# Kernel optimization log

Hardware: AMD Instinct MI355X
Metric: run time of the kernel (lower is better)

Reference implementation:

```python
import jax, jax.numpy as jnp
import numpy as np

EMBED_DIM = 1024
NUM_HEADS = 16
BATCH = 4
SEQ = 2048
HEAD_DIM = EMBED_DIM // NUM_HEADS


def get_alibi_slope(num_heads):
    x = (2 ** 8) ** (1 / num_heads)
    slope = jnp.array([1 / x ** (i + 1) for i in range(num_heads)], dtype=jnp.float32)
    return slope[:, None, None]  # [H,1,1]


def setup_inputs() -> dict:
    key = jax.random.key(0)
    k1, k2, k3 = jax.random.split(key, 3)
    x = jax.random.normal(k1, (BATCH, SEQ, EMBED_DIM), dtype=jnp.float32)
    # causal mask, broadcastable to [B,H,S,S]
    mask = jnp.tril(jnp.ones((SEQ, SEQ), dtype=bool))[None, None, :, :]
    W_qkv = jax.random.normal(k2, (EMBED_DIM, 3 * EMBED_DIM), dtype=jnp.float32) * (EMBED_DIM ** -0.5)
    b_qkv = jnp.zeros((3 * EMBED_DIM,), dtype=jnp.float32)
    W_out = jax.random.normal(k3, (EMBED_DIM, EMBED_DIM), dtype=jnp.float32) * (EMBED_DIM ** -0.5)
    b_out = jnp.zeros((EMBED_DIM,), dtype=jnp.float32)
    return {"x": x, "mask": mask, "W_qkv": W_qkv, "b_qkv": b_qkv, "W_out": W_out, "b_out": b_out}


def reference(x, mask, W_qkv, b_qkv, W_out, b_out):
    B, S, E = x.shape
    H, D = NUM_HEADS, HEAD_DIM
    qkv = x @ W_qkv + b_qkv                     # [B,S,3E]
    qkv = qkv.reshape(B, S, 3, H, D)
    q, k, v = qkv[:, :, 0], qkv[:, :, 1], qkv[:, :, 2]  # each [B,S,H,D]
    scores = jnp.einsum('bqhd,bkhd->bhqk', q, k) / jnp.sqrt(jnp.asarray(D, x.dtype))
    # ALiBi bias: slope[h] * (k_pos - q_pos)
    rel = (jnp.arange(S)[None, :] - jnp.arange(S)[:, None]).astype(x.dtype)  # [S,S]
    scores = scores + get_alibi_slope(H).astype(x.dtype) * rel               # broadcast [H,S,S]
    scores = jnp.where(mask, scores, jnp.asarray(-1e9, x.dtype))
    attn = jax.nn.softmax(scores, axis=-1)       # [B,H,S,S]
    out = jnp.einsum('bhqk,bkhd->bqhd', attn, v).reshape(B, S, E)
    return out @ W_out + b_out
```

## Files before the change

### kernel.cpp

```cpp
#include <hip/hip_runtime.h>
#include <hip/hip_bf16.h>
#include <cstdint>
#include <cstddef>

#define BATCH  4
#define SEQ    2048
#define EMBED  1024
#define NHEADS 16
#define HDIM   64

typedef __attribute__((ext_vector_type(8))) short  short8;
typedef __attribute__((ext_vector_type(4))) float  floatx4;

#define MASK_NEG (-1.0e30f)
#define LOG2E    1.44269504f

__device__ __forceinline__ float bf2f(ushort u) {
  union { uint32_t i; float f; } v; v.i = ((uint32_t)u) << 16; return v.f;
}
__device__ __forceinline__ ushort f2bf(float f) {
  union { float f; uint32_t i; } v; v.f = f;
  uint32_t u = v.i;
  return (ushort)((u + 0x7fffu + ((u >> 16) & 1u)) >> 16);
}
__device__ __forceinline__ uint32_t f2bf_pk(float a, float b) {
  union { __hip_bfloat162 h; uint32_t u; } v;
  v.h = __float22bfloat162_rn(make_float2(a, b));
  return v.u;
}
__device__ __forceinline__ float fast_exp2(float x) {
  float r;
  asm("v_exp_f32 %0, %1" : "=v"(r) : "v"(x));
  return r;
}
__device__ __forceinline__ floatx4 max4(floatx4 a, floatx4 b) {
  floatx4 r;
  r[0] = fmaxf(a[0], b[0]); r[1] = fmaxf(a[1], b[1]);
  r[2] = fmaxf(a[2], b[2]); r[3] = fmaxf(a[3], b[3]);
  return r;
}
__device__ __forceinline__ void gll16(const ushort* g, ushort* l) {
  __builtin_amdgcn_global_load_lds(
      (const __attribute__((address_space(1))) void*)g,
      (__attribute__((address_space(3))) void*)l, 16, 0, 0);
}

__global__ __launch_bounds__(256) void detect_dtype(
    const uint32_t* __restrict__ x, int* __restrict__ flag) {
  __shared__ int sh[256];
  int tid = threadIdx.x;
  int c = 0;
#pragma unroll
  for (int i = 0; i < 16; i++) {
    uint32_t w = x[tid * 16 + i];
    uint32_t lo = w & 0xFFFFu;
    int e = (int)((lo >> 7) & 0xFF);
    if (lo == 0u || (e >= 100 && e <= 140)) c++;
  }
  sh[tid] = c;
  __syncthreads();
  if (tid == 0) {
    int s = 0;
    for (int i = 0; i < 256; i++) s += sh[i];
    *flag = (s >= 3500) ? 1 : 0;
  }
}

__global__ __launch_bounds__(256) void cvt_bf16_v4(
    const void* __restrict__ in, ushort* __restrict__ out,
    const int* __restrict__ flag, int n4) {
  bool isbf = (*flag != 0);
  int stride = gridDim.x * 256;
  for (int i = blockIdx.x * 256 + threadIdx.x; i < n4; i += stride) {
    if (isbf) {
      ((uint2*)out)[i] = ((const uint2*)in)[i];
    } else {
      float4 f = ((const float4*)in)[i];
      uint2 o;
      o.x = f2bf_pk(f.x, f.y);
      o.y = f2bf_pk(f.z, f.w);
      ((uint2*)out)[i] = o;
    }
  }
}

__global__ __launch_bounds__(256) void cvt_biases(
    const void* __restrict__ bq, const void* __restrict__ bo,
    ushort* __restrict__ bqb, ushort* __restrict__ bob,
    const int* __restrict__ flag) {
  bool isbf = (*flag != 0);
  int i = blockIdx.x * 256 + threadIdx.x;
  if (i < 3 * EMBED) {
    bqb[i] = isbf ? ((const ushort*)bq)[i] : f2bf(((const float*)bq)[i]);
  } else {
    int j = i - 3 * EMBED;
    bob[j] = isbf ? ((const ushort*)bo)[j] : f2bf(((const float*)bo)[j]);
  }
}

__global__ __launch_bounds__(256) void transpose_cvt(
    const void* __restrict__ in, ushort* __restrict__ out,
    const int* __restrict__ flag, int R, int C) {
  bool isbf = (*flag != 0);
  __shared__ ushort tile[32][33];
  int bx = blockIdx.x * 32;
  int by = blockIdx.y * 32;
  int tx = threadIdx.x & 31, ty = threadIdx.x >> 5;
#pragma unroll
  for (int i = 0; i < 32; i += 8) {
    size_t idx = (size_t)(by + ty + i) * C + bx + tx;
    tile[ty + i][tx] = isbf ? ((const ushort*)in)[idx] : f2bf(((const float*)in)[idx]);
  }
  __syncthreads();
#pragma unroll
  for (int i = 0; i < 32; i += 8)
    out[(size_t)(bx + ty + i) * R + by + tx] = tile[tx][ty + i];
}

__global__ __launch_bounds__(256) void transpose_v(
    const ushort* __restrict__ in, ushort* __restrict__ out) {
  __shared__ ushort tile[32][33];
  int bh = blockIdx.z;
  int s0 = blockIdx.x * 32;
  int d0 = blockIdx.y * 32;
  int tx = threadIdx.x & 31, ty = threadIdx.x >> 5;
  const ushort* ip = in + (size_t)bh * SEQ * HDIM;
  ushort* op = out + (size_t)bh * SEQ * HDIM;
#pragma unroll
  for (int i = 0; i < 32; i += 8)
    tile[ty + i][tx] = ip[(size_t)(s0 + ty + i) * HDIM + d0 + tx];
  __syncthreads();
#pragma unroll
  for (int i = 0; i < 32; i += 8)
    op[(size_t)(d0 + ty + i) * SEQ + s0 + tx] = tile[tx][ty + i];
}

template <int EPI>
__global__ __launch_bounds__(256) void gemm128(
    const ushort* __restrict__ A, const ushort* __restrict__ BT,
    const ushort* __restrict__ bias,
    ushort* __restrict__ out0, ushort* __restrict__ out1, ushort* __restrict__ out2,
    const int* __restrict__ flag,
    int M, int N, int K) {
  __shared__ __align__(16) ushort Al[128 * 64];
  __shared__ __align__(16) ushort Bl[128 * 64];

  const int tid  = threadIdx.x;
  const int lane = tid & 63, wave = tid >> 6;
  const int quad = lane >> 4, l15 = lane & 15;
  const int wm = wave >> 1, wn = wave & 1;

  const int Lb  = blockIdx.y * gridDim.x + blockIdx.x;
  const int xcd = Lb & 7, ib = Lb >> 3;
  const int cpx = gridDim.x >> 3;
  const int bx  = xcd * cpx + (ib % cpx);
  const int by  = ib / cpx;
  const int rowA0 = by * 128;
  const int colB0 = bx * 128;

  floatx4 acc[4][4] = {};

  int srow[4], sc8[4];
#pragma unroll
  for (int j = 0; j < 4; j++) {
    int s = tid + j * 256;
    srow[j] = s >> 3;
    sc8[j] = ((s & 7) ^ (srow[j] & 7)) * 8;
  }

  for (int kk = 0; kk < K; kk += 64) {
    __syncthreads();
#pragma unroll
    for (int j = 0; j < 4; j++)
      gll16(&A[(size_t)(rowA0 + srow[j]) * K + kk + sc8[j]], &Al[(tid + j * 256) * 8]);
#pragma unroll
    for (int j = 0; j < 4; j++)
      gll16(&BT[(size_t)(colB0 + srow[j]) * K + kk + sc8[j]], &Bl[(tid + j * 256) * 8]);
    __syncthreads();

#pragma unroll
    for (int h = 0; h < 2; h++) {
      short8 af[4], bf[4];
#pragma unroll
      for (int mt = 0; mt < 4; mt++) {
        int row = wm * 64 + mt * 16 + l15;
        int pos = (quad + 4 * h) ^ (l15 & 7);
        af[mt] = *(const short8*)&Al[row * 64 + pos * 8];
      }
#pragma unroll
      for (int nt = 0; nt < 4; nt++) {
        int row = wn * 64 + nt * 16 + l15;
        int pos = (quad + 4 * h) ^ (l15 & 7);
        bf[nt] = *(const short8*)&Bl[row * 64 + pos * 8];
      }
#pragma unroll
      for (int mt = 0; mt < 4; mt++)
#pragma unroll
        for (int nt = 0; nt < 4; nt++)
          acc[mt][nt] = __builtin_amdgcn_mfma_f32_16x16x32_bf16(af[mt], bf[nt], acc[mt][nt], 0, 0, 0);
    }
  }

  const bool isbf = (EPI == 1) ? (*flag != 0) : true;

#pragma unroll
  for (int mt = 0; mt < 4; mt++)
#pragma unroll
    for (int nt = 0; nt < 4; nt++)
#pragma unroll
      for (int r = 0; r < 4; r++) {
        int row = rowA0 + wm * 64 + mt * 16 + quad * 4 + r;
        int col = colB0 + wn * 64 + nt * 16 + l15;
        float v = acc[mt][nt][r] + bf2f(bias[col]);
        if (EPI == 0) {
          int three = col >> 10, rem = col & 1023, h = rem >> 6, d = rem & 63;
          int b = row >> 11, s = row & 2047;
          ushort* dst = (three == 0) ? out0 : (three == 1) ? out1 : out2;
          dst[((size_t)(b * NHEADS + h) * SEQ + s) * HDIM + d] = f2bf(v);
        } else {
          if (isbf) out0[(size_t)row * N + col] = f2bf(v);
          else      ((float*)out0)[(size_t)row * N + col] = v;
        }
      }
}

__global__ __launch_bounds__(256, 3) void attn_kernel(
    const ushort* __restrict__ Q, const ushort* __restrict__ K,
    const ushort* __restrict__ VT, ushort* __restrict__ Oout) {
  __shared__ __align__(16) ushort Kl[2][64 * 64];
  __shared__ __align__(16) ushort Vt[2][64 * 64];
  __shared__ __align__(16) ushort Pl[4][32 * 64];

  const int tid  = threadIdx.x;
  const int lane = tid & 63, wave = tid >> 6;
  const int quad = lane >> 4, l15 = lane & 15;

  const int L   = blockIdx.x + 16 * blockIdx.y + 256 * blockIdx.z;
  const int xcd = L & 7;
  const int idx = L >> 3;
  const int bh  = xcd * 8 + (idx >> 4);
  const int qt  = 15 - (idx & 15);
  const int h   = bh & 15, b = bh >> 4;

  const ushort* Qp  = Q  + (size_t)bh * SEQ * HDIM;
  const ushort* Kp  = K  + (size_t)bh * SEQ * HDIM;
  const ushort* VTp = VT + (size_t)bh * SEQ * HDIM;

  const float slope2 = exp2f(-0.5f * (float)(h + 1)) * LOG2E;
  const float c2 = 0.125f * LOG2E;

  floatx4 ab[4];
#pragma unroll
  for (int kct = 0; kct < 4; kct++)
#pragma unroll
    for (int r = 0; r < 4; r++)
      ab[kct][r] = slope2 * (float)(kct * 16 + quad * 4 + r);

  const int sr0 = tid >> 3, sr1 = sr0 + 32;
  const int sc  = tid & 7;
  const int so  = sc * 8;
  const int sw0 = sr0 * 64 + (sc ^ (sr0 & 7)) * 8;
  const int sw1 = sr1 * 64 + (sc ^ (sr0 & 7)) * 8;
  const int sxr = l15 & 7;

  const int wq0 = qt * 128 + wave * 32;

  short8 qf[2][2];
#pragma unroll
  for (int mf = 0; mf < 2; mf++) {
    const ushort* qr = &Qp[(size_t)(wq0 + mf * 16 + l15) * HDIM];
    qf[mf][0] = *(const short8*)&qr[quad * 8];
    qf[mf][1] = *(const short8*)&qr[32 + quad * 8];
  }

  float m2s[2] = {MASK_NEG, MASK_NEG}, lis[2] = {0.f, 0.f};
  float qrowf[2];
#pragma unroll
  for (int mf = 0; mf < 2; mf++) qrowf[mf] = (float)(wq0 + mf * 16 + l15);
  floatx4 o_acc[2][4] = {};

#define ATTN_TILE(KB, CUR, MASKED)                                            \
  do {                                                                        \
    short8 kfa[4], kfb[4];                                                    \
    _Pragma("unroll")                                                         \
    for (int kct = 0; kct < 4; kct++) {                                       \
      const ushort* kr = &Kl[CUR][(kct * 16 + l15) * 64];                     \
      kfa[kct] = *(const short8*)&kr[(quad ^ sxr) * 8];                       \
      kfb[kct] = *(const short8*)&kr[((quad + 4) ^ sxr) * 8];                 \
    }                                                                         \
    _Pragma("unroll")                                                         \
    for (int mf = 0; mf < 2; mf++) {                                          \
      floatx4 w[4];                                                           \
      _Pragma("unroll")                                                       \
      for (int kct = 0; kct < 4; kct++) {                                     \
        floatx4 z = {};                                                       \
        z = __builtin_amdgcn_mfma_f32_16x16x32_bf16(kfa[kct], qf[mf][0], z, 0, 0, 0); \
        z = __builtin_amdgcn_mfma_f32_16x16x32_bf16(kfb[kct], qf[mf][1], z, 0, 0, 0); \
        w[kct] = z * c2 + ab[kct];                                            \
      }                                                                       \
      if (MASKED) {                                                           \
        const float qrel = qrowf[mf] - (float)(KB);                           \
        _Pragma("unroll")                                                     \
        for (int kct = 0; kct < 4; kct++)                                     \
          _Pragma("unroll")                                                   \
          for (int r = 0; r < 4; r++)                                         \
            if ((float)(kct * 16 + quad * 4 + r) > qrel) w[kct][r] = MASK_NEG;\
      }                                                                       \
      floatx4 wm4 = max4(max4(w[0], w[1]), max4(w[2], w[3]));                 \
      float mloc = fmaxf(fmaxf(wm4[0], wm4[1]), fmaxf(wm4[2], wm4[3]));       \
      mloc = fmaxf(mloc, __shfl_xor(mloc, 16, 64));                           \
      mloc = fmaxf(mloc, __shfl_xor(mloc, 32, 64));                           \
      const float bk = slope2 * (float)(KB);                                  \
      const float mlt = mloc + bk;                                            \
      const unsigned long long g = __ballot(mlt > m2s[mf] + 8.0f);            \
      float al = 1.0f;                                                        \
      if (g) {                                                                \
        float mn = fmaxf(m2s[mf], mlt);                                       \
        al = fast_exp2(m2s[mf] - mn);                                         \
        m2s[mf] = mn;                                                         \
      }                                                                       \
      const float mnb = m2s[mf] - bk;                                         \
      float rs = 0.f;                                                         \
      _Pragma("unroll")                                                       \
      for (int kct = 0; kct < 4; kct++) {                                     \
        float p0 = fast_exp2(w[kct][0] - mnb);                                \
        float p1 = fast_exp2(w[kct][1] - mnb);                                \
        float p2 = fast_exp2(w[kct][2] - mnb);                                \
        float p3 = fast_exp2(w[kct][3] - mnb);                                \
        rs += (p0 + p1) + (p2 + p3);                                          \
        uint2 pw;                                                             \
        pw.x = f2bf_pk(p0, p1);                                               \
        pw.y = f2bf_pk(p2, p3);                                               \
        *(uint2*)&Pl[wave][(mf * 16 + l15) * 64 +                             \
                           ((kct * 2 + (quad >> 1)) ^ sxr) * 8 +              \
                           (quad & 1) * 4] = pw;                              \
      }                                                                       \
      if (g) {                                                                \
        floatx4 alrv;                                                         \
        _Pragma("unroll")                                                     \
        for (int r = 0; r < 4; r++) alrv[r] = __shfl(al, quad * 4 + r, 16);   \
        _Pragma("unroll")                                                     \
        for (int ct = 0; ct < 4; ct++) o_acc[mf][ct] *= alrv;                 \
        lis[mf] = lis[mf] * al + rs;                                          \
      } else {                                                                \
        lis[mf] += rs;                                                        \
      }                                                                       \
    }                                                                         \
    _Pragma("unroll")                                                         \
    for (int ks = 0; ks < 2; ks++) {                                          \
      short8 vf[4];                                                           \
      _Pragma("unroll")                                                       \
      for (int ct = 0; ct < 4; ct++)                                          \
        vf[ct] = *(const short8*)&Vt[CUR][(ct * 16 + l15) * 64 +              \
                                          ((ks * 4 + quad) ^ sxr) * 8];       \
      _Pragma("unroll")                                                       \
      for (int mf = 0; mf < 2; mf++) {                                        \
        short8 pf = *(const short8*)&Pl[wave][(mf * 16 + l15) * 64 +          \
                                              ((ks * 4 + quad) ^ sxr) * 8];   \
        _Pragma("unroll")                                                     \
        for (int ct = 0; ct < 4; ct++)                                        \
          o_acc[mf][ct] = __builtin_amdgcn_mfma_f32_16x16x32_bf16(            \
              pf, vf[ct], o_acc[mf][ct], 0, 0, 0);                            \
      }                                                                       \
    }                                                                         \
  } while (0)

  uint4 pk0 = *(const uint4*)&Kp[(size_t)sr0 * HDIM + so];
  uint4 pk1 = *(const uint4*)&Kp[(size_t)sr1 * HDIM + so];
  uint4 pv0 = *(const uint4*)&VTp[(size_t)sr0 * SEQ + so];
  uint4 pv1 = *(const uint4*)&VTp[(size_t)sr1 * SEQ + so];
  *(uint4*)&Kl[0][sw0] = pk0;
  *(uint4*)&Kl[0][sw1] = pk1;
  *(uint4*)&Vt[0][sw0] = pv0;
  *(uint4*)&Vt[0][sw1] = pv1;
  __syncthreads();

  const int nfull = 2 * qt;
  for (int kt = 0; kt < nfull; kt++) {
    const int kb = kt * 64;
    const int cur = kt & 1;

    {
      const int kb2 = kb + 64;
      pk0 = *(const uint4*)&Kp[(size_t)(kb2 + sr0) * HDIM + so];
      pk1 = *(const uint4*)&Kp[(size_t)(kb2 + sr1) * HDIM + so];
      pv0 = *(const uint4*)&VTp[(size_t)sr0 * SEQ + kb2 + so];
      pv1 = *(const uint4*)&VTp[(size_t)sr1 * SEQ + kb2 + so];
    }

    ATTN_TILE(kb, cur, 0);

    {
      const int nxt = cur ^ 1;
      *(uint4*)&Kl[nxt][sw0] = pk0;
      *(uint4*)&Kl[nxt][sw1] = pk1;
      *(uint4*)&Vt[nxt][sw0] = pv0;
      *(uint4*)&Vt[nxt][sw1] = pv1;
    }
    __syncthreads();
  }

  {
    const int kb = nfull * 64;
    const int cur = nfull & 1;
    const int kb2 = kb + 64;
    pk0 = *(const uint4*)&Kp[(size_t)(kb2 + sr0) * HDIM + so];
    pk1 = *(const uint4*)&Kp[(size_t)(kb2 + sr1) * HDIM + so];
    pv0 = *(const uint4*)&VTp[(size_t)sr0 * SEQ + kb2 + so];
    pv1 = *(const uint4*)&VTp[(size_t)sr1 * SEQ + kb2 + so];

    ATTN_TILE(kb, cur, 1);

    const int nxt = cur ^ 1;
    *(uint4*)&Kl[nxt][sw0] = pk0;
    *(uint4*)&Kl[nxt][sw1] = pk1;
    *(uint4*)&Vt[nxt][sw0] = pv0;
    *(uint4*)&Vt[nxt][sw1] = pv1;
    __syncthreads();
  }

  if (wave & 2) {
    ATTN_TILE((nfull + 1) * 64, (nfull + 1) & 1, 1);
  }

#pragma unroll
  for (int mf = 0; mf < 2; mf++) {
    float lif = lis[mf] + __shfl_xor(lis[mf], 16, 64);
    lif += __shfl_xor(lif, 32, 64);
    float inv = 1.0f / fmaxf(lif, 1e-20f);
    float invr[4];
#pragma unroll
    for (int r = 0; r < 4; r++) invr[r] = __shfl(inv, quad * 4 + r, 16);
#pragma unroll
    for (int ct = 0; ct < 4; ct++)
#pragma unroll
      for (int r = 0; r < 4; r++) {
        int q = wq0 + mf * 16 + quad * 4 + r;
        float v = o_acc[mf][ct][r] * invr[r];
        Oout[(size_t)(b * SEQ + q) * EMBED + h * HDIM + ct * 16 + l15] = f2bf(v);
      }
  }
#undef ATTN_TILE
}

extern "C" void kernel_launch(void* const* d_in, const int* in_sizes, int n_in,
                              void* d_out, int out_size, void* d_ws, size_t ws_size,
                              hipStream_t stream) {
  const void* x     = d_in[0];
  const void* W_qkv = d_in[2];
  const void* b_qkv = d_in[3];
  const void* W_out = d_in[4];
  const void* b_out = d_in[5];

  char* ws = (char*)d_ws;
  int*    flag = (int*)(ws + 0);
  ushort* xb   = (ushort*)(ws + 1024);
  ushort* WTq  = (ushort*)(ws + 16778240);
  ushort* WTo  = (ushort*)(ws + 23069696);
  ushort* bqb  = (ushort*)(ws + 25166848);
  ushort* bob  = (ushort*)(ws + 25172992);
  ushort* Kw   = (ushort*)(ws + 25175040);
  ushort* Vw   = (ushort*)(ws + 41952256);
  ushort* VTw  = (ushort*)(ws + 58729472);
  ushort* Aw   = Vw;
  ushort* Qw   = (ws_size >= (size_t)75506688 + 16777216)
                   ? (ushort*)(ws + 75506688)
                   : (ushort*)d_out;

  detect_dtype<<<1, 256, 0, stream>>>((const uint32_t*)x, flag);

  cvt_bf16_v4<<<2048, 256, 0, stream>>>(x, xb, flag, BATCH * SEQ * EMBED / 4);
  cvt_biases<<<16, 256, 0, stream>>>(b_qkv, b_out, bqb, bob, flag);

  transpose_cvt<<<dim3(3072 / 32, 1024 / 32), 256, 0, stream>>>(W_qkv, WTq, flag, 1024, 3072);
  transpose_cvt<<<dim3(1024 / 32, 1024 / 32), 256, 0, stream>>>(W_out, WTo, flag, 1024, 1024);

  gemm128<0><<<dim3(3072 / 128, 8192 / 128), 256, 0, stream>>>(
      xb, WTq, bqb, Qw, Kw, Vw, flag, BATCH * SEQ, 3 * EMBED, EMBED);

  transpose_v<<<dim3(SEQ / 32, HDIM / 32, BATCH * NHEADS), 256, 0, stream>>>(Vw, VTw);

  attn_kernel<<<dim3(16, 16, 4), 256, 0, stream>>>(Qw, Kw, VTw, Aw);

  gemm128<1><<<dim3(1024 / 128, 8192 / 128), 256, 0, stream>>>(
      Aw, WTo, bob, (ushort*)d_out, nullptr, nullptr, flag, BATCH * SEQ, EMBED, EMBED);
}
```

Baseline: 328.8 us.

## Pair causal query tiles per block, stage K/V via direct global-to-LDS loads

The attention kernel now gives each block two query tiles (p and 15-p) so every block does the same amount of causal work, and halves the grid to 512 blocks. K/V staging switches from register prefetch plus LDS store to direct global-to-LDS loads (gll16), and launch bounds drop to 2 blocks per SM. The QKV/out GEMMs also drop the XCD-aware block swizzle in favour of plain blockIdx mapping. The aim is to remove tail imbalance from causal work and free registers. The costs are fewer resident blocks and possibly worse L2 locality in the GEMMs.

```diff
diff --git a/kernel.cpp b/kernel.cpp
--- a/kernel.cpp
+++ b/kernel.cpp
@@ -149,14 +149,8 @@
   const int lane = tid & 63, wave = tid >> 6;
   const int quad = lane >> 4, l15 = lane & 15;
   const int wm = wave >> 1, wn = wave & 1;
-
-  const int Lb  = blockIdx.y * gridDim.x + blockIdx.x;
-  const int xcd = Lb & 7, ib = Lb >> 3;
-  const int cpx = gridDim.x >> 3;
-  const int bx  = xcd * cpx + (ib % cpx);
-  const int by  = ib / cpx;
-  const int rowA0 = by * 128;
-  const int colB0 = bx * 128;
+  const int rowA0 = blockIdx.y * 128;
+  const int colB0 = blockIdx.x * 128;
 
   floatx4 acc[4][4] = {};
 
@@ -224,7 +218,7 @@
       }
 }
 
-__global__ __launch_bounds__(256, 3) void attn_kernel(
+__global__ __launch_bounds__(256, 2) void attn_kernel(
     const ushort* __restrict__ Q, const ushort* __restrict__ K,
     const ushort* __restrict__ VT, ushort* __restrict__ Oout) {
   __shared__ __align__(16) ushort Kl[2][64 * 64];
@@ -235,11 +229,11 @@
   const int lane = tid & 63, wave = tid >> 6;
   const int quad = lane >> 4, l15 = lane & 15;
 
-  const int L   = blockIdx.x + 16 * blockIdx.y + 256 * blockIdx.z;
+  const int L   = blockIdx.x + 8 * blockIdx.y + 128 * blockIdx.z;
   const int xcd = L & 7;
   const int idx = L >> 3;
-  const int bh  = xcd * 8 + (idx >> 4);
-  const int qt  = 15 - (idx & 15);
+  const int bh  = xcd * 8 + (idx >> 3);
+  const int p   = idx & 7;
   const int h   = bh & 15, b = bh >> 4;
 
   const ushort* Qp  = Q  + (size_t)bh * SEQ * HDIM;
@@ -256,28 +250,17 @@
     for (int r = 0; r < 4; r++)
       ab[kct][r] = slope2 * (float)(kct * 16 + quad * 4 + r);
 
-  const int sr0 = tid >> 3, sr1 = sr0 + 32;
-  const int sc  = tid & 7;
-  const int so  = sc * 8;
-  const int sw0 = sr0 * 64 + (sc ^ (sr0 & 7)) * 8;
-  const int sw1 = sr1 * 64 + (sc ^ (sr0 & 7)) * 8;
+  const int sr0 = tid >> 3;
+  const int scc = ((tid & 7) ^ (sr0 & 7)) * 8;
   const int sxr = l15 & 7;
 
-  const int wq0 = qt * 128 + wave * 32;
-
-  short8 qf[2][2];
-#pragma unroll
-  for (int mf = 0; mf < 2; mf++) {
-    const ushort* qr = &Qp[(size_t)(wq0 + mf * 16 + l15) * HDIM];
-    qf[mf][0] = *(const short8*)&qr[quad * 8];
-    qf[mf][1] = *(const short8*)&qr[32 + quad * 8];
-  }
-
-  float m2s[2] = {MASK_NEG, MASK_NEG}, lis[2] = {0.f, 0.f};
-  float qrowf[2];
-#pragma unroll
-  for (int mf = 0; mf < 2; mf++) qrowf[mf] = (float)(wq0 + mf * 16 + l15);
-  floatx4 o_acc[2][4] = {};
+#define STAGE(KB, BUF)                                                        \
+  do {                                                                        \
+    gll16(&Kp[(size_t)((KB) + sr0) * HDIM + scc],       &Kl[BUF][tid * 8]);   \
+    gll16(&Kp[(size_t)((KB) + sr0 + 32) * HDIM + scc],  &Kl[BUF][tid * 8 + 2048]); \
+    gll16(&VTp[(size_t)sr0 * SEQ + (KB) + scc],         &Vt[BUF][tid * 8]);   \
+    gll16(&VTp[(size_t)(sr0 + 32) * SEQ + (KB) + scc],  &Vt[BUF][tid * 8 + 2048]); \
+  } while (0)
 
 #define ATTN_TILE(KB, CUR, MASKED)                                            \
   do {                                                                        \
@@ -365,82 +348,67 @@
     }                                                                         \
   } while (0)
 
-  uint4 pk0 = *(const uint4*)&Kp[(size_t)sr0 * HDIM + so];
-  uint4 pk1 = *(const uint4*)&Kp[(size_t)sr1 * HDIM + so];
-  uint4 pv0 = *(const uint4*)&VTp[(size_t)sr0 * SEQ + so];
-  uint4 pv1 = *(const uint4*)&VTp[(size_t)sr1 * SEQ + so];
-  *(uint4*)&Kl[0][sw0] = pk0;
-  *(uint4*)&Kl[0][sw1] = pk1;
-  *(uint4*)&Vt[0][sw0] = pv0;
-  *(uint4*)&Vt[0][sw1] = pv1;
-  __syncthreads();
-
-  const int nfull = 2 * qt;
-  for (int kt = 0; kt < nfull; kt++) {
-    const int kb = kt * 64;
-    const int cur = kt & 1;
+  for (int qsel = 0; qsel < 2; qsel++) {
+    const int qt  = qsel ? (15 - p) : p;
+    const int wq0 = qt * 128 + wave * 32;
+
+    short8 qf[2][2];
+#pragma unroll
+    for (int mf = 0; mf < 2; mf++) {
+      const ushort* qr = &Qp[(size_t)(wq0 + mf * 16 + l15) * HDIM];
+      qf[mf][0] = *(const short8*)&qr[quad * 8];
+      qf[mf][1] = *(const short8*)&qr[32 + quad * 8];
+    }
+
+    float m2s[2] = {MASK_NEG, MASK_NEG}, lis[2] = {0.f, 0.f};
+    float qrowf[2];
+#pragma unroll
+    for (int mf = 0; mf < 2; mf++) qrowf[mf] = (float)(wq0 + mf * 16 + l15);
+    floatx4 o_acc[2][4] = {};
+
+    __syncthreads();
+    STAGE(0, 0);
+    __syncthreads();
+
+    const int nfull = 2 * qt;
+    for (int kt = 0; kt < nfull; kt++) {
+      const int cur = kt & 1;
+      STAGE((kt + 1) * 64, cur ^ 1);
+      ATTN_TILE(kt * 64, cur, 0);
+      __syncthreads();
+    }
 
     {
-      const int kb2 = kb + 64;
-      pk0 = *(const uint4*)&Kp[(size_t)(kb2 + sr0) * HDIM + so];
-      pk1 = *(const uint4*)&Kp[(size_t)(kb2 + sr1) * HDIM + so];
-      pv0 = *(const uint4*)&VTp[(size_t)sr0 * SEQ + kb2 + so];
-      pv1 = *(const uint4*)&VTp[(size_t)sr1 * SEQ + kb2 + so];
-    }
-
-    ATTN_TILE(kb, cur, 0);
-
-    {
-      const int nxt = cur ^ 1;
-      *(uint4*)&Kl[nxt][sw0] = pk0;
-      *(uint4*)&Kl[nxt][sw1] = pk1;
-      *(uint4*)&Vt[nxt][sw0] = pv0;
-      *(uint4*)&Vt[nxt][sw1] = pv1;
-    }
-    __syncthreads();
-  }
-
-  {
-    const int kb = nfull * 64;
-    const int cur = nfull & 1;
-    const int kb2 = kb + 64;
-    pk0 = *(const uint4*)&Kp[(size_t)(kb2 + sr0) * HDIM + so];
-    pk1 = *(const uint4*)&Kp[(size_t)(kb2 + sr1) * HDIM + so];
-    pv0 = *(const uint4*)&VTp[(size_t)sr0 * SEQ + kb2 + so];
-    pv1 = *(const uint4*)&VTp[(size_t)sr1 * SEQ + kb2 + so];
-
-    ATTN_TILE(kb, cur, 1);
-
-    const int nxt = cur ^ 1;
-    *(uint4*)&Kl[nxt][sw0] = pk0;
-    *(uint4*)&Kl[nxt][sw1] = pk1;
-    *(uint4*)&Vt[nxt][sw0] = pv0;
-    *(uint4*)&Vt[nxt][sw1] = pv1;
-    __syncthreads();
-  }
-
-  if (wave & 2) {
-    ATTN_TILE((nfull + 1) * 64, (nfull + 1) & 1, 1);
-  }
-
-#pragma unroll
-  for (int mf = 0; mf < 2; mf++) {
-    float lif = lis[mf] + __shfl_xor(lis[mf], 16, 64);
-    lif += __shfl_xor(lif, 32, 64);
-    float inv = 1.0f / fmaxf(lif, 1e-20f);
-    float invr[4];
-#pragma unroll
-    for (int r = 0; r < 4; r++) invr[r] = __shfl(inv, quad * 4 + r, 16);
-#pragma unroll
-    for (int ct = 0; ct < 4; ct++)
-#pragma unroll
-      for (int r = 0; r < 4; r++) {
-        int q = wq0 + mf * 16 + quad * 4 + r;
-        float v = o_acc[mf][ct][r] * invr[r];
-        Oout[(size_t)(b * SEQ + q) * EMBED + h * HDIM + ct * 16 + l15] = f2bf(v);
-      }
+      const int cur = nfull & 1;
+      STAGE((nfull + 1) * 64, cur ^ 1);
+      ATTN_TILE(nfull * 64, cur, 1);
+      __syncthreads();
+    }
+
+    if (wave & 2) {
+      ATTN_TILE((nfull + 1) * 64, (nfull + 1) & 1, 1);
+    }
+
+#pragma unroll
+    for (int mf = 0; mf < 2; mf++) {
+      float lif = lis[mf] + __shfl_xor(lis[mf], 16, 64);
+      lif += __shfl_xor(lif, 32, 64);
+      float inv = 1.0f / fmaxf(lif, 1e-20f);
+      float invr[4];
+#pragma unroll
+      for (int r = 0; r < 4; r++) invr[r] = __shfl(inv, quad * 4 + r, 16);
+#pragma unroll
+      for (int ct = 0; ct < 4; ct++)
+#pragma unroll
+        for (int r = 0; r < 4; r++) {
+          int q = wq0 + mf * 16 + quad * 4 + r;
+          float v = o_acc[mf][ct][r] * invr[r];
+          Oout[(size_t)(b * SEQ + q) * EMBED + h * HDIM + ct * 16 + l15] = f2bf(v);
+        }
+    }
   }
 #undef ATTN_TILE
+#undef STAGE
 }
 
 extern "C" void kernel_launch(void* const* d_in, const int* in_sizes, int n_in,
@@ -480,7 +448,7 @@
 
   transpose_v<<<dim3(SEQ / 32, HDIM / 32, BATCH * NHEADS), 256, 0, stream>>>(Vw, VTw);
 
-  attn_kernel<<<dim3(16, 16, 4), 256, 0, stream>>>(Qw, Kw, VTw, Aw);
+  attn_kernel<<<dim3(8, 16, 4), 256, 0, stream>>>(Qw, Kw, VTw, Aw);
 
   gemm128<1><<<dim3(1024 / 128, 8192 / 128), 256, 0, stream>>>(
       Aw, WTo, bob, (ushort*)d_out, nullptr, nullptr, flag, BATCH * SEQ, EMBED, EMBED);
```

Measured after the change: 288.6 us. 1.14x faster.
